# Kernel tuning notes

Measured on AMD Instinct MI355X. Metric: run time of the kernel, lower is better.

Reference implementation:

```python
import jax, jax.numpy as jnp
import numpy as np

GRID = 16
K = 2
NW = (GRID - K + 1) ** 2  # 225 sliding 2x2 windows on the 16x16 grid


def _make_mask():
    idx = np.arange(GRID * GRID).reshape(GRID, GRID)
    wins = np.stack([idx[i:i + K, j:j + K].ravel()
                     for i in range(GRID - K + 1) for j in range(GRID - K + 1)])
    m = np.zeros((NW, GRID * GRID), np.float32)
    m[np.arange(NW)[:, None], wins] = 1.0
    return jnp.asarray(m)

MASK = _make_mask()          # [225, 256] window -> covered cells
MASK_COUNT = MASK.sum(0)     # windows covering each cell
BN_SCALE = np.float32(1.0 / np.sqrt(1.0 + 1e-5))  # eval BN, running mean=0 var=1


def _adapter(x, w1, w2):
    return jax.nn.relu(jax.nn.relu(x @ w1.T) @ w2.T)


def _bn(x, g, b):
    return x * (g * BN_SCALE) + b


def _head(x, w1, b1, g2, be2, w2, b2, g3, be3, w3, b3):
    x = _bn(jax.nn.relu(x @ w1.T + b1), g2, be2)
    x = _bn(jax.nn.relu(x @ w2.T + b2), g3, be3)
    return jax.nn.sigmoid(x @ w3.T + b3)[:, 0]


def setup_inputs() -> dict:
    B, L, P, D, R, S = 64, 3, 225, 640, 1800, 240
    key = jax.random.key(0)
    ks = jax.random.split(key, 16)
    n = lambda k, s, sc=1.0: jax.random.normal(k, s, jnp.float32) * sc
    te = n(ks[3], (2, D)); te = te / jnp.linalg.norm(te, axis=-1, keepdims=True)
    pr = n(ks[5], (L, R, D)); pr = pr / jnp.linalg.norm(pr, axis=-1, keepdims=True)
    w = 0.05
    return dict(
        image=n(ks[0], (B, 3, S, S)),
        image_embeds=n(ks[1], (B, D)),
        patch_embeds=n(ks[2], (L, B, P, D)),
        text_embeds=te,
        image_embeds_ref=n(ks[4], (1, D)),
        patch_embeds_ref=pr,
        a_w1=n(ks[6], (160, D), w), a_w2=n(ks[7], (D, 160), w),
        r_w1=n(ks[8], (128, D), w), r_b1=jnp.zeros((128,)),
        r_g2=jnp.ones((128,)), r_be2=jnp.zeros((128,)),
        r_w2=n(ks[9], (64, 128), w), r_b2=jnp.zeros((64,)),
        r_g3=jnp.ones((64,)), r_be3=jnp.zeros((64,)),
        r_w3=n(ks[10], (1, 64), w), r_b3=jnp.zeros((1,)),
        h_w1=n(ks[11], (128, P), w), h_b1=jnp.zeros((128,)),
        h_g2=jnp.ones((128,)), h_be2=jnp.zeros((128,)),
        h_w2=n(ks[12], (64, 128), w), h_b2=jnp.zeros((64,)),
        h_g3=jnp.ones((64,)), h_be3=jnp.zeros((64,)),
        h_w3=n(ks[13], (1, 64), w), h_b3=jnp.zeros((1,)),
    )


def reference(image, image_embeds, patch_embeds, text_embeds, image_embeds_ref,
              patch_embeds_ref, a_w1, a_w2,
              r_w1, r_b1, r_g2, r_be2, r_w2, r_b2, r_g3, r_be3, r_w3, r_b3,
              h_w1, h_b1, h_g2, h_be2, h_w2, h_b2, h_g3, h_be3, h_w3, h_b3):
    pe = patch_embeds / jnp.linalg.norm(patch_embeds, axis=-1, keepdims=True)
    nie = image_embeds / jnp.linalg.norm(image_embeds, axis=-1, keepdims=True)
    text_score = jax.nn.softmax(100.0 * nie @ text_embeds.T, axis=-1)[:, 1]
    # kNN-style min-distance over reference patches: [L,B,P,R]
    sim = jnp.einsum('lbpd,lrd->lbpr', pe, patch_embeds_ref)
    patch_ref_map = ((1.0 - sim).min(axis=3) / 2.0).mean(axis=0)  # [B,P]
    fg_score = patch_ref_map.max(axis=1)
    diff = image_embeds_ref - _adapter(image_embeds, a_w1, a_w2)
    img_ref_score = _head(diff, r_w1, r_b1, r_g2, r_be2, r_w2, r_b2, r_g3, r_be3, r_w3, r_b3)
    holistic = (text_score + img_ref_score)[:, None] + patch_ref_map  # [B,225]
    hl_score = _head(holistic, h_w1, h_b1, h_g2, h_be2, h_w2, h_b2, h_g3, h_be3, h_w3, h_b3)
    final_score = (hl_score + fg_score) / 2.0
    # harmonic aggregation of window scores onto the 16x16 grid
    heat = (MASK_COUNT / ((1.0 / holistic) @ MASK)).reshape(-1, GRID, GRID)
    hmap = jax.image.resize(heat, (heat.shape[0], image.shape[2], image.shape[3]), 'bilinear')
    return final_score, hmap
```

## Files before the change

kernel.cpp:

```cpp
#include <hip/hip_runtime.h>
#include <stdint.h>
#include <math.h>

#define L_DIM 3
#define B_DIM 64
#define P_DIM 225
#define D_DIM 640
#define R_DIM 1800
#define S_DIM 240
#define M_TOT 14400
#define M_PAD 14592
#define N_PAD 2048
#define MT 57
#define NT 8
#define KT 10
#define BNSCALE 0.99999500003749981f

typedef __bf16 bf16x8 __attribute__((ext_vector_type(8)));
typedef float f32x4 __attribute__((ext_vector_type(4)));

__device__ __forceinline__ unsigned short f2bf(float f) {
    union { float f; unsigned u; } v; v.f = f;
    unsigned u = v.u;
    unsigned r = (u + 0x7FFFu + ((u >> 16) & 1u)) >> 16;
    return (unsigned short)r;
}

__global__ __launch_bounds__(256)
void k_convert(const float* __restrict__ pe, const float* __restrict__ per,
               unsigned short* __restrict__ abf, unsigned short* __restrict__ rbf,
               float* __restrict__ rnorm)
{
    const int AROWS = L_DIM * M_PAD;
    int wid = (blockIdx.x * 256 + threadIdx.x) >> 6;
    int lane = threadIdx.x & 63;
    const ushort4 z4 = {0, 0, 0, 0};
    if (wid < AROWS) {
        int l = wid / M_PAD, r = wid - l * M_PAD;
        unsigned short* dst = abf + (size_t)wid * D_DIM;
        if (r < M_TOT) {
            const float4* src = (const float4*)(pe + ((size_t)l * M_TOT + r) * D_DIM);
            float ss = 0.f;
            #pragma unroll
            for (int it = 0; it < 3; ++it) {
                int idx = it * 64 + lane;
                if (idx < 160) {
                    float4 v = src[idx];
                    ss += v.x * v.x + v.y * v.y + v.z * v.z + v.w * v.w;
                    ushort4 o;
                    o.x = f2bf(v.x); o.y = f2bf(v.y); o.z = f2bf(v.z); o.w = f2bf(v.w);
                    *(ushort4*)(dst + idx * 4) = o;
                }
            }
            #pragma unroll
            for (int m = 32; m; m >>= 1) ss += __shfl_xor(ss, m);
            if (lane == 0) rnorm[l * M_TOT + r] = rsqrtf(ss);
        } else {
            #pragma unroll
            for (int it = 0; it < 3; ++it) {
                int idx = it * 64 + lane;
                if (idx < 160) *(ushort4*)(dst + idx * 4) = z4;
            }
        }
    } else {
        int w2 = wid - AROWS;
        int l = w2 / N_PAD, r = w2 - l * N_PAD;
        unsigned short* dst = rbf + (size_t)w2 * D_DIM;
        if (r < R_DIM) {
            const float4* src = (const float4*)(per + ((size_t)l * R_DIM + r) * D_DIM);
            #pragma unroll
            for (int it = 0; it < 3; ++it) {
                int idx = it * 64 + lane;
                if (idx < 160) {
                    float4 v = src[idx];
                    ushort4 o;
                    o.x = f2bf(v.x); o.y = f2bf(v.y); o.z = f2bf(v.z); o.w = f2bf(v.w);
                    *(ushort4*)(dst + idx * 4) = o;
                }
            }
        } else {
            #pragma unroll
            for (int it = 0; it < 3; ++it) {
                int idx = it * 64 + lane;
                if (idx < 160) *(ushort4*)(dst + idx * 4) = z4;
            }
        }
    }
}

#define MFMA(A, B, C) __builtin_amdgcn_mfma_f32_16x16x32_bf16((A), (B), (C), 0, 0, 0)
#define GLL(SRC, DSTOFF)                                                     \
    __builtin_amdgcn_global_load_lds(                                        \
        (const __attribute__((address_space(1))) void*)(SRC),               \
        (__attribute__((address_space(3))) void*)(lds + (DSTOFF)), 16, 0, 0)

#define RD_BQ(D0, D1, D2, D3, Q, BASE) do {                                  \
    D0 = *(const bf16x8*)(lds + (BASE) + (brow0 + (Q) * 32) * 64 + sw0);     \
    D1 = *(const bf16x8*)(lds + (BASE) + (brow0 + (Q) * 32) * 64 + sw1);     \
    D2 = *(const bf16x8*)(lds + (BASE) + (brow0 + (Q) * 32 + 16) * 64 + sw0);\
    D3 = *(const bf16x8*)(lds + (BASE) + (brow0 + (Q) * 32 + 16) * 64 + sw1);\
} while (0)

#define RD_A(BASE) do { _Pragma("unroll")                                    \
    for (int mi = 0; mi < 4; ++mi) {                                         \
        a[mi][0] = *(const bf16x8*)(lds + (BASE) + (arow0 + mi * 16) * 64 + sw0); \
        a[mi][1] = *(const bf16x8*)(lds + (BASE) + (arow0 + mi * 16) * 64 + sw1); \
    } } while (0)

#define MM(NJB, B0, B1, B2, B3) do { _Pragma("unroll")                       \
    for (int mi = 0; mi < 4; ++mi) {                                         \
        acc[mi][NJB]     = MFMA(a[mi][0], B0, acc[mi][NJB]);                 \
        acc[mi][NJB]     = MFMA(a[mi][1], B1, acc[mi][NJB]);                 \
        acc[mi][NJB + 1] = MFMA(a[mi][0], B2, acc[mi][NJB + 1]);             \
        acc[mi][NJB + 1] = MFMA(a[mi][1], B3, acc[mi][NJB + 1]);             \
    } } while (0)

__global__ __launch_bounds__(512, 2)
void k_gemm_max(const unsigned short* __restrict__ abf,
                const unsigned short* __restrict__ rbf,
                float* __restrict__ pmax)
{
    __shared__ unsigned short lds[65536];
    __shared__ float red[2][256];

    int bid = blockIdx.x;
    int v = (bid & 7) * 171 + (bid >> 3);
    int l = v / (MT * NT);
    int rem = v - l * (MT * NT);
    int mt = rem >> 3;
    int nt = rem & 7;

    int tid = threadIdx.x;
    int wid = tid >> 6, lane = tid & 63;
    int wm = wid >> 1;
    int wn = wid & 1;
    int lane15 = lane & 15, lg = lane >> 4;
    int sA = lane15 & 7;
    int sw0 = ((lg) ^ sA) << 3;
    int sw1 = ((4 + lg) ^ sA) << 3;
    int arow0 = wm * 64 + lane15;
    int brow0 = wn * 128 + lane15;

    int rowc = lane >> 3;
    int scol = ((lane & 7) ^ rowc) << 3;
    const unsigned short* gA = abf + (size_t)(l * M_PAD + mt * 256) * D_DIM;
    const unsigned short* gB = rbf + (size_t)(l * N_PAD + nt * 256) * D_DIM;
    int chA0 = wid, chA1 = 8 + wid, chA2 = 16 + wid, chA3 = 24 + wid;
    int chB0 = (wid < 4) ? (0 + wid) : (12 + wid);
    int chB1 = (wid < 4) ? (4 + wid) : (16 + wid);
    int chB2 = (wid < 4) ? (8 + wid) : (20 + wid);
    int chB3 = (wid < 4) ? (12 + wid) : (24 + wid);
    const unsigned short* pA0 = gA + (size_t)(chA0 * 8 + rowc) * D_DIM + scol;
    const unsigned short* pA1 = gA + (size_t)(chA1 * 8 + rowc) * D_DIM + scol;
    const unsigned short* pA2 = gA + (size_t)(chA2 * 8 + rowc) * D_DIM + scol;
    const unsigned short* pA3 = gA + (size_t)(chA3 * 8 + rowc) * D_DIM + scol;
    const unsigned short* pB0 = gB + (size_t)(chB0 * 8 + rowc) * D_DIM + scol;
    const unsigned short* pB1 = gB + (size_t)(chB1 * 8 + rowc) * D_DIM + scol;
    const unsigned short* pB2 = gB + (size_t)(chB2 * 8 + rowc) * D_DIM + scol;
    const unsigned short* pB3 = gB + (size_t)(chB3 * 8 + rowc) * D_DIM + scol;

    f32x4 acc[4][8];
    #pragma unroll
    for (int mi = 0; mi < 4; ++mi)
        #pragma unroll
        for (int nj = 0; nj < 8; ++nj)
            acc[mi][nj] = f32x4{0.f, 0.f, 0.f, 0.f};

    GLL(pA0, chA0 * 512); GLL(pA1, chA1 * 512);
    GLL(pA2, chA2 * 512); GLL(pA3, chA3 * 512);
    GLL(pB0, 32768 + chB0 * 512); GLL(pB1, 32768 + chB1 * 512);
    GLL(pB2, 32768 + chB2 * 512); GLL(pB3, 32768 + chB3 * 512);
    asm volatile("s_waitcnt vmcnt(3)" ::: "memory");
    __builtin_amdgcn_s_barrier();

    bf16x8 a[4][2];
    bf16x8 ba0, ba1, ba2, ba3, bb0, bb1, bb2, bb3;
    RD_A(0);
    RD_BQ(ba0, ba1, ba2, ba3, 0, 32768);

    int buf = 0;
    for (int kt = 0; kt < KT; ++kt) {
        int ob = buf ^ 1;
        int bB = 32768 + buf * 16384;
        int oaB = ob * 16384;
        int obB = 32768 + ob * 16384;
        int koff = (kt + 1 < KT ? kt + 1 : KT - 1) * 64;

        GLL(pA0 + koff, oaB + chA0 * 512); GLL(pA1 + koff, oaB + chA1 * 512);
        asm volatile("s_waitcnt vmcnt(4)" ::: "memory");
        __builtin_amdgcn_s_barrier();
        RD_BQ(bb0, bb1, bb2, bb3, 1, bB);
        __builtin_amdgcn_s_setprio(1);
        MM(0, ba0, ba1, ba2, ba3);
        __builtin_amdgcn_s_setprio(0);

        GLL(pA2 + koff, oaB + chA2 * 512); GLL(pA3 + koff, oaB + chA3 * 512);
        asm volatile("s_waitcnt vmcnt(5)" ::: "memory");
        __builtin_amdgcn_s_barrier();
        RD_BQ(ba0, ba1, ba2, ba3, 2, bB);
        __builtin_amdgcn_s_setprio(1);
        MM(2, bb0, bb1, bb2, bb3);
        __builtin_amdgcn_s_setprio(0);

        GLL(pB0 + koff, obB + chB0 * 512); GLL(pB1 + koff, obB + chB1 * 512);
        asm volatile("s_waitcnt vmcnt(6)" ::: "memory");
        __builtin_amdgcn_s_barrier();
        RD_BQ(bb0, bb1, bb2, bb3, 3, bB);
        __builtin_amdgcn_s_setprio(1);
        MM(4, ba0, ba1, ba2, ba3);
        __builtin_amdgcn_s_setprio(0);

        GLL(pB2 + koff, obB + chB2 * 512); GLL(pB3 + koff, obB + chB3 * 512);
        asm volatile("s_waitcnt vmcnt(3)" ::: "memory");
        __builtin_amdgcn_s_barrier();
        RD_A(oaB);
        RD_BQ(ba0, ba1, ba2, ba3, 0, obB);
        __builtin_amdgcn_s_setprio(1);
        MM(6, bb0, bb1, bb2, bb3);
        __builtin_amdgcn_s_setprio(0);

        buf = ob;
    }

    __syncthreads();

    int colbase = nt * 256 + wn * 128 + lane15;
    #pragma unroll
    for (int mi = 0; mi < 4; ++mi) {
        float t[4] = {-__builtin_inff(), -__builtin_inff(),
                      -__builtin_inff(), -__builtin_inff()};
        #pragma unroll
        for (int nj = 0; nj < 8; ++nj) {
            if (colbase + nj * 16 < R_DIM) {
                #pragma unroll
                for (int r = 0; r < 4; ++r) t[r] = fmaxf(t[r], acc[mi][nj][r]);
            }
        }
        #pragma unroll
        for (int m = 1; m <= 8; m <<= 1) {
            #pragma unroll
            for (int r = 0; r < 4; ++r) t[r] = fmaxf(t[r], __shfl_xor(t[r], m));
        }
        if (lane15 == 0) {
            int rb = wm * 64 + mi * 16 + lg * 4;
            #pragma unroll
            for (int r = 0; r < 4; ++r) red[wn][rb + r] = t[r];
        }
    }
    __syncthreads();
    if (tid < 256) {
        float vmx = fmaxf(red[0][tid], red[1][tid]);
        pmax[((size_t)l * NT + nt) * M_PAD + mt * 256 + tid] = vmx;
    }
}

__device__ __forceinline__ float block_sum8(float v, volatile float* scratch) {
    #pragma unroll
    for (int m = 32; m; m >>= 1) v += __shfl_xor(v, m);
    int w = threadIdx.x >> 6;
    __syncthreads();
    if ((threadIdx.x & 63) == 0) scratch[w] = v;
    __syncthreads();
    float r = 0.f;
    #pragma unroll
    for (int i = 0; i < 8; ++i) r += scratch[i];
    return r;
}
__device__ __forceinline__ float block_max8(float v, volatile float* scratch) {
    #pragma unroll
    for (int m = 32; m; m >>= 1) v = fmaxf(v, __shfl_xor(v, m));
    int w = threadIdx.x >> 6;
    __syncthreads();
    if ((threadIdx.x & 63) == 0) scratch[w] = v;
    __syncthreads();
    float r = scratch[0];
    #pragma unroll
    for (int i = 1; i < 8; ++i) r = fmaxf(r, scratch[i]);
    return r;
}

__global__ __launch_bounds__(512)
void k_small(const float* __restrict__ ie, const float* __restrict__ te,
             const float* __restrict__ ier,
             const float* __restrict__ a_w1, const float* __restrict__ a_w2,
             const float* __restrict__ r_w1, const float* __restrict__ r_b1,
             const float* __restrict__ r_g2, const float* __restrict__ r_be2,
             const float* __restrict__ r_w2, const float* __restrict__ r_b2,
             const float* __restrict__ r_g3, const float* __restrict__ r_be3,
             const float* __restrict__ r_w3, const float* __restrict__ r_b3,
             const float* __restrict__ h_w1, const float* __restrict__ h_b1,
             const float* __restrict__ h_g2, const float* __restrict__ h_be2,
             const float* __restrict__ h_w2, const float* __restrict__ h_b2,
             const float* __restrict__ h_g3, const float* __restrict__ h_be3,
             const float* __restrict__ h_w3, const float* __restrict__ h_b3,
             const float* __restrict__ pmax, const float* __restrict__ rnorm,
             float* __restrict__ heat, float* __restrict__ out_score)
{
    int b = blockIdx.x, tid = threadIdx.x;
    __shared__ float x[D_DIM];
    __shared__ float h1[160];
    __shared__ float dif[D_DIM];
    __shared__ float z1[128];
    __shared__ float z2[64];
    __shared__ float hol[P_DIM];
    __shared__ float rcp[P_DIM];
    __shared__ float scratch[8];

    for (int i = tid; i < D_DIM; i += 512) x[i] = ie[b * D_DIM + i];
    __syncthreads();

    float ss = 0.f, d0 = 0.f, d1 = 0.f;
    for (int i = tid; i < D_DIM; i += 512) {
        float v = x[i];
        ss += v * v;
        d0 += v * te[i];
        d1 += v * te[D_DIM + i];
    }
    float ssum = block_sum8(ss, scratch);
    float dd0 = block_sum8(d0, scratch);
    float dd1 = block_sum8(d1, scratch);
    float tscore = 1.f / (1.f + expf(100.f * rsqrtf(ssum) * (dd0 - dd1)));

    for (int o = tid; o < 160; o += 512) {
        const float* w = a_w1 + (size_t)o * D_DIM;
        float s0 = 0, s1 = 0, s2 = 0, s3 = 0;
        for (int d = 0; d < D_DIM; d += 4) {
            s0 += x[d] * w[d]; s1 += x[d + 1] * w[d + 1];
            s2 += x[d + 2] * w[d + 2]; s3 += x[d + 3] * w[d + 3];
        }
        h1[o] = fmaxf((s0 + s1) + (s2 + s3), 0.f);
    }
    __syncthreads();
    for (int d = tid; d < D_DIM; d += 512) {
        const float* w = a_w2 + (size_t)d * 160;
        float s0 = 0, s1 = 0, s2 = 0, s3 = 0;
        for (int o = 0; o < 160; o += 4) {
            s0 += h1[o] * w[o]; s1 += h1[o + 1] * w[o + 1];
            s2 += h1[o + 2] * w[o + 2]; s3 += h1[o + 3] * w[o + 3];
        }
        dif[d] = ier[d] - fmaxf((s0 + s1) + (s2 + s3), 0.f);
    }
    __syncthreads();

    for (int o = tid; o < 128; o += 512) {
        const float* w = r_w1 + (size_t)o * D_DIM;
        float s0 = 0, s1 = 0, s2 = 0, s3 = 0;
        for (int d = 0; d < D_DIM; d += 4) {
            s0 += dif[d] * w[d]; s1 += dif[d + 1] * w[d + 1];
            s2 += dif[d + 2] * w[d + 2]; s3 += dif[d + 3] * w[d + 3];
        }
        float s = (s0 + s1) + (s2 + s3) + r_b1[o];
        z1[o] = fmaxf(s, 0.f) * (r_g2[o] * BNSCALE) + r_be2[o];
    }
    __syncthreads();
    for (int o = tid; o < 64; o += 512) {
        const float* w = r_w2 + (size_t)o * 128;
        float s = r_b2[o];
        for (int d = 0; d < 128; ++d) s += z1[d] * w[d];
        z2[o] = fmaxf(s, 0.f) * (r_g3[o] * BNSCALE) + r_be3[o];
    }
    __syncthreads();
    float sp = (tid < 64) ? z2[tid] * r_w3[tid] : 0.f;
    float irs = 1.f / (1.f + expf(-(block_sum8(sp, scratch) + r_b3[0])));

    float fgp = -__builtin_inff();
    float base = tscore + irs;
    for (int p = tid; p < P_DIM; p += 512) {
        int r = b * P_DIM + p;
        float s = 0.f;
        #pragma unroll
        for (int l = 0; l < L_DIM; ++l) {
            float m = -__builtin_inff();
            #pragma unroll
            for (int t = 0; t < NT; ++t)
                m = fmaxf(m, pmax[((size_t)l * NT + t) * M_PAD + r]);
            s += m * rnorm[l * M_TOT + r];
        }
        float pv = (3.0f - s) / 6.0f;
        fgp = fmaxf(fgp, pv);
        float h = base + pv;
        hol[p] = h;
        rcp[p] = 1.f / h;
    }
    float fg = block_max8(fgp, scratch);

    for (int o = tid; o < 128; o += 512) {
        const float* w = h_w1 + (size_t)o * P_DIM;
        float s = h_b1[o];
        for (int d = 0; d < P_DIM; ++d) s += hol[d] * w[d];
        z1[o] = fmaxf(s, 0.f) * (h_g2[o] * BNSCALE) + h_be2[o];
    }
    __syncthreads();
    for (int o = tid; o < 64; o += 512) {
        const float* w = h_w2 + (size_t)o * 128;
        float s = h_b2[o];
        for (int d = 0; d < 128; ++d) s += z1[d] * w[d];
        z2[o] = fmaxf(s, 0.f) * (h_g3[o] * BNSCALE) + h_be3[o];
    }
    __syncthreads();
    float sp2 = (tid < 64) ? z2[tid] * h_w3[tid] : 0.f;
    float hl_in = block_sum8(sp2, scratch) + h_b3[0];
    if (tid == 0) {
        float hl = 1.f / (1.f + expf(-hl_in));
        out_score[b] = (hl + fg) * 0.5f;
    }

    if (tid < 256) {
        int r = tid >> 4, c = tid & 15;
        float s = 0.f, cnt = 0.f;
        #pragma unroll
        for (int di = -1; di <= 0; ++di) {
            int i = r + di;
            if (i < 0 || i > 14) continue;
            #pragma unroll
            for (int dj = -1; dj <= 0; ++dj) {
                int j = c + dj;
                if (j < 0 || j > 14) continue;
                s += rcp[i * 15 + j];
                cnt += 1.f;
            }
        }
        heat[b * 256 + tid] = cnt / s;
    }
}

__global__ __launch_bounds__(256)
void k_resize(const float* __restrict__ heat, float* __restrict__ outh)
{
    int b = blockIdx.x >> 3, sub = blockIdx.x & 7;
    __shared__ float h[256];
    if (threadIdx.x < 256) h[threadIdx.x] = heat[b * 256 + threadIdx.x];
    __syncthreads();
    int base = sub * 30 * S_DIM;
    for (int q = threadIdx.x; q < 30 * S_DIM; q += 256) {
        int px = base + q;
        int y = px / S_DIM, xc = px - y * S_DIM;
        float sy = fminf(fmaxf((y - 7) * (1.0f / 15.0f), 0.f), 15.f);
        float sx = fminf(fmaxf((xc - 7) * (1.0f / 15.0f), 0.f), 15.f);
        int y0 = (int)sy, x0 = (int)sx;
        int y1 = min(y0 + 1, 15), x1 = min(x0 + 1, 15);
        float fy = sy - (float)y0, fx = sx - (float)x0;
        float v00 = h[y0 * 16 + x0], v01 = h[y0 * 16 + x1];
        float v10 = h[y1 * 16 + x0], v11 = h[y1 * 16 + x1];
        float v = (1.f - fy) * ((1.f - fx) * v00 + fx * v01)
                + fy * ((1.f - fx) * v10 + fx * v11);
        outh[(size_t)b * (S_DIM * S_DIM) + px] = v;
    }
}

extern "C" void kernel_launch(void* const* d_in, const int* in_sizes, int n_in,
                              void* d_out, int out_size, void* d_ws, size_t ws_size,
                              hipStream_t stream)
{
    (void)in_sizes; (void)n_in; (void)out_size; (void)ws_size;
    const float* image_embeds = (const float*)d_in[1];
    const float* patch_embeds = (const float*)d_in[2];
    const float* text_embeds  = (const float*)d_in[3];
    const float* ier          = (const float*)d_in[4];
    const float* per          = (const float*)d_in[5];
    const float* a_w1 = (const float*)d_in[6];
    const float* a_w2 = (const float*)d_in[7];
    const float* r_w1 = (const float*)d_in[8];
    const float* r_b1 = (const float*)d_in[9];
    const float* r_g2 = (const float*)d_in[10];
    const float* r_be2 = (const float*)d_in[11];
    const float* r_w2 = (const float*)d_in[12];
    const float* r_b2 = (const float*)d_in[13];
    const float* r_g3 = (const float*)d_in[14];
    const float* r_be3 = (const float*)d_in[15];
    const float* r_w3 = (const float*)d_in[16];
    const float* r_b3 = (const float*)d_in[17];
    const float* h_w1 = (const float*)d_in[18];
    const float* h_b1 = (const float*)d_in[19];
    const float* h_g2 = (const float*)d_in[20];
    const float* h_be2 = (const float*)d_in[21];
    const float* h_w2 = (const float*)d_in[22];
    const float* h_b2 = (const float*)d_in[23];
    const float* h_g3 = (const float*)d_in[24];
    const float* h_be3 = (const float*)d_in[25];
    const float* h_w3 = (const float*)d_in[26];
    const float* h_b3 = (const float*)d_in[27];

    char* ws = (char*)d_ws;
    size_t off = 0;
    auto take = [&](size_t bytes) -> void* {
        void* p = ws + off;
        off += (bytes + 255) & ~(size_t)255;
        return p;
    };
    float* rnorm = (float*)take((size_t)L_DIM * M_TOT * 4);
    float* pmax  = (float*)take((size_t)L_DIM * NT * M_PAD * 4);
    float* heat  = (float*)take((size_t)B_DIM * 256 * 4);
    unsigned short* abf = (unsigned short*)take((size_t)L_DIM * M_PAD * D_DIM * 2);
    unsigned short* rbf = (unsigned short*)take((size_t)L_DIM * N_PAD * D_DIM * 2);

    float* out_f = (float*)d_out;

    k_convert<<<dim3((L_DIM * M_PAD + L_DIM * N_PAD) / 4), dim3(256), 0, stream>>>(
        patch_embeds, per, abf, rbf, rnorm);
    k_gemm_max<<<dim3(L_DIM * MT * NT), dim3(512), 0, stream>>>(abf, rbf, pmax);
    k_small<<<dim3(B_DIM), dim3(512), 0, stream>>>(image_embeds, text_embeds, ier,
        a_w1, a_w2, r_w1, r_b1, r_g2, r_be2, r_w2, r_b2, r_g3, r_be3, r_w3, r_b3,
        h_w1, h_b1, h_g2, h_be2, h_w2, h_b2, h_g3, h_be3, h_w3, h_b3,
        pmax, rnorm, heat, out_f);
    k_resize<<<dim3(B_DIM * 8), dim3(256), 0, stream>>>(heat, out_f + B_DIM);
}
```

Before: 212.4 us.

## Restructure GEMM k-loop into two half-stages and fuse resize into k_small

```diff
diff --git a/kernel.cpp b/kernel.cpp
--- a/kernel.cpp
+++ b/kernel.cpp
@@ -94,11 +94,11 @@
         (const __attribute__((address_space(1))) void*)(SRC),               \
         (__attribute__((address_space(3))) void*)(lds + (DSTOFF)), 16, 0, 0)
 
-#define RD_BQ(D0, D1, D2, D3, Q, BASE) do {                                  \
-    D0 = *(const bf16x8*)(lds + (BASE) + (brow0 + (Q) * 32) * 64 + sw0);     \
-    D1 = *(const bf16x8*)(lds + (BASE) + (brow0 + (Q) * 32) * 64 + sw1);     \
-    D2 = *(const bf16x8*)(lds + (BASE) + (brow0 + (Q) * 32 + 16) * 64 + sw0);\
-    D3 = *(const bf16x8*)(lds + (BASE) + (brow0 + (Q) * 32 + 16) * 64 + sw1);\
+#define RD_Q(D, Q, BASE) do {                                                \
+    D[0] = *(const bf16x8*)(lds + (BASE) + (brow0 + (Q) * 32) * 64 + sw0);   \
+    D[1] = *(const bf16x8*)(lds + (BASE) + (brow0 + (Q) * 32) * 64 + sw1);   \
+    D[2] = *(const bf16x8*)(lds + (BASE) + (brow0 + (Q) * 32 + 16) * 64 + sw0); \
+    D[3] = *(const bf16x8*)(lds + (BASE) + (brow0 + (Q) * 32 + 16) * 64 + sw1); \
 } while (0)
 
 #define RD_A(BASE) do { _Pragma("unroll")                                    \
@@ -107,15 +107,15 @@
         a[mi][1] = *(const bf16x8*)(lds + (BASE) + (arow0 + mi * 16) * 64 + sw1); \
     } } while (0)
 
-#define MM(NJB, B0, B1, B2, B3) do { _Pragma("unroll")                       \
+#define MM(NJB, BQ) do { _Pragma("unroll")                                   \
     for (int mi = 0; mi < 4; ++mi) {                                         \
-        acc[mi][NJB]     = MFMA(a[mi][0], B0, acc[mi][NJB]);                 \
-        acc[mi][NJB]     = MFMA(a[mi][1], B1, acc[mi][NJB]);                 \
-        acc[mi][NJB + 1] = MFMA(a[mi][0], B2, acc[mi][NJB + 1]);             \
-        acc[mi][NJB + 1] = MFMA(a[mi][1], B3, acc[mi][NJB + 1]);             \
+        acc[mi][NJB]     = MFMA(a[mi][0], BQ[0], acc[mi][NJB]);              \
+        acc[mi][NJB]     = MFMA(a[mi][1], BQ[1], acc[mi][NJB]);              \
+        acc[mi][NJB + 1] = MFMA(a[mi][0], BQ[2], acc[mi][NJB + 1]);          \
+        acc[mi][NJB + 1] = MFMA(a[mi][1], BQ[3], acc[mi][NJB + 1]);          \
     } } while (0)
 
-__global__ __launch_bounds__(512, 2)
+__global__ __launch_bounds__(512, 1)
 void k_gemm_max(const unsigned short* __restrict__ abf,
                 const unsigned short* __restrict__ rbf,
                 float* __restrict__ pmax)
@@ -170,56 +170,62 @@
     GLL(pA2, chA2 * 512); GLL(pA3, chA3 * 512);
     GLL(pB0, 32768 + chB0 * 512); GLL(pB1, 32768 + chB1 * 512);
     GLL(pB2, 32768 + chB2 * 512); GLL(pB3, 32768 + chB3 * 512);
-    asm volatile("s_waitcnt vmcnt(3)" ::: "memory");
+    asm volatile("s_waitcnt vmcnt(2)" ::: "memory");
     __builtin_amdgcn_s_barrier();
 
-    bf16x8 a[4][2];
-    bf16x8 ba0, ba1, ba2, ba3, bb0, bb1, bb2, bb3;
-    RD_A(0);
-    RD_BQ(ba0, ba1, ba2, ba3, 0, 32768);
-
     int buf = 0;
-    for (int kt = 0; kt < KT; ++kt) {
+    for (int kt = 0; kt < KT - 1; ++kt) {
         int ob = buf ^ 1;
+        int aB = buf * 16384;
         int bB = 32768 + buf * 16384;
         int oaB = ob * 16384;
         int obB = 32768 + ob * 16384;
-        int koff = (kt + 1 < KT ? kt + 1 : KT - 1) * 64;
-
-        GLL(pA0 + koff, oaB + chA0 * 512); GLL(pA1 + koff, oaB + chA1 * 512);
-        asm volatile("s_waitcnt vmcnt(4)" ::: "memory");
+        int koff = (kt + 1) * 64;
+
+        bf16x8 a[4][2];
+        {
+            RD_A(aB);
+            bf16x8 q0[4], q1[4];
+            RD_Q(q0, 0, bB); RD_Q(q1, 1, bB);
+            GLL(pA0 + koff, oaB + chA0 * 512); GLL(pA1 + koff, oaB + chA1 * 512);
+            GLL(pA2 + koff, oaB + chA2 * 512); GLL(pA3 + koff, oaB + chA3 * 512);
+            asm volatile("s_waitcnt vmcnt(4)" ::: "memory");
+            __builtin_amdgcn_s_barrier();
+            __builtin_amdgcn_s_setprio(1);
+            MM(0, q0); MM(2, q1);
+            __builtin_amdgcn_s_setprio(0);
+        }
+        {
+            bf16x8 q2[4], q3[4];
+            RD_Q(q2, 2, bB); RD_Q(q3, 3, bB);
+            GLL(pB0 + koff, obB + chB0 * 512); GLL(pB1 + koff, obB + chB1 * 512);
+            GLL(pB2 + koff, obB + chB2 * 512); GLL(pB3 + koff, obB + chB3 * 512);
+            asm volatile("s_waitcnt vmcnt(2)" ::: "memory");
+            __builtin_amdgcn_s_barrier();
+            __builtin_amdgcn_s_setprio(1);
+            MM(4, q2); MM(6, q3);
+            __builtin_amdgcn_s_setprio(0);
+        }
+        buf = ob;
+    }
+
+    {
+        int aB = buf * 16384;
+        int bB = 32768 + buf * 16384;
+        bf16x8 a[4][2];
+        RD_A(aB);
+        bf16x8 q0[4], q1[4];
+        RD_Q(q0, 0, bB); RD_Q(q1, 1, bB);
+        asm volatile("s_waitcnt vmcnt(0)" ::: "memory");
         __builtin_amdgcn_s_barrier();
-        RD_BQ(bb0, bb1, bb2, bb3, 1, bB);
         __builtin_amdgcn_s_setprio(1);
-        MM(0, ba0, ba1, ba2, ba3);
+        MM(0, q0); MM(2, q1);
         __builtin_amdgcn_s_setprio(0);
-
-        GLL(pA2 + koff, oaB + chA2 * 512); GLL(pA3 + koff, oaB + chA3 * 512);
-        asm volatile("s_waitcnt vmcnt(5)" ::: "memory");
-        __builtin_amdgcn_s_barrier();
-        RD_BQ(ba0, ba1, ba2, ba3, 2, bB);
+        bf16x8 q2[4], q3[4];
+        RD_Q(q2, 2, bB); RD_Q(q3, 3, bB);
         __builtin_amdgcn_s_setprio(1);
-        MM(2, bb0, bb1, bb2, bb3);
+        MM(4, q2); MM(6, q3);
         __builtin_amdgcn_s_setprio(0);
-
-        GLL(pB0 + koff, obB + chB0 * 512); GLL(pB1 + koff, obB + chB1 * 512);
-        asm volatile("s_waitcnt vmcnt(6)" ::: "memory");
-        __builtin_amdgcn_s_barrier();
-        RD_BQ(bb0, bb1, bb2, bb3, 3, bB);
-        __builtin_amdgcn_s_setprio(1);
-        MM(4, ba0, ba1, ba2, ba3);
-        __builtin_amdgcn_s_setprio(0);
-
-        GLL(pB2 + koff, obB + chB2 * 512); GLL(pB3 + koff, obB + chB3 * 512);
-        asm volatile("s_waitcnt vmcnt(3)" ::: "memory");
-        __builtin_amdgcn_s_barrier();
-        RD_A(oaB);
-        RD_BQ(ba0, ba1, ba2, ba3, 0, obB);
-        __builtin_amdgcn_s_setprio(1);
-        MM(6, bb0, bb1, bb2, bb3);
-        __builtin_amdgcn_s_setprio(0);
-
-        buf = ob;
     }
 
     __syncthreads();
@@ -294,7 +300,7 @@
              const float* __restrict__ h_g3, const float* __restrict__ h_be3,
              const float* __restrict__ h_w3, const float* __restrict__ h_b3,
              const float* __restrict__ pmax, const float* __restrict__ rnorm,
-             float* __restrict__ heat, float* __restrict__ out_score)
+             float* __restrict__ out_score, float* __restrict__ outh)
 {
     int b = blockIdx.x, tid = threadIdx.x;
     __shared__ float x[D_DIM];
@@ -304,6 +310,7 @@
     __shared__ float z2[64];
     __shared__ float hol[P_DIM];
     __shared__ float rcp[P_DIM];
+    __shared__ float heatl[256];
     __shared__ float scratch[8];
 
     for (int i = tid; i < D_DIM; i += 512) x[i] = ie[b * D_DIM + i];
@@ -420,31 +427,23 @@
                 cnt += 1.f;
             }
         }
-        heat[b * 256 + tid] = cnt / s;
-    }
-}
-
-__global__ __launch_bounds__(256)
-void k_resize(const float* __restrict__ heat, float* __restrict__ outh)
-{
-    int b = blockIdx.x >> 3, sub = blockIdx.x & 7;
-    __shared__ float h[256];
-    if (threadIdx.x < 256) h[threadIdx.x] = heat[b * 256 + threadIdx.x];
-    __syncthreads();
-    int base = sub * 30 * S_DIM;
-    for (int q = threadIdx.x; q < 30 * S_DIM; q += 256) {
-        int px = base + q;
+        heatl[tid] = cnt / s;
+    }
+    __syncthreads();
+
+    float* dst = outh + (size_t)b * (S_DIM * S_DIM);
+    for (int px = tid; px < S_DIM * S_DIM; px += 512) {
         int y = px / S_DIM, xc = px - y * S_DIM;
         float sy = fminf(fmaxf((y - 7) * (1.0f / 15.0f), 0.f), 15.f);
         float sx = fminf(fmaxf((xc - 7) * (1.0f / 15.0f), 0.f), 15.f);
         int y0 = (int)sy, x0 = (int)sx;
         int y1 = min(y0 + 1, 15), x1 = min(x0 + 1, 15);
         float fy = sy - (float)y0, fx = sx - (float)x0;
-        float v00 = h[y0 * 16 + x0], v01 = h[y0 * 16 + x1];
-        float v10 = h[y1 * 16 + x0], v11 = h[y1 * 16 + x1];
-        float v = (1.f - fy) * ((1.f - fx) * v00 + fx * v01)
-                + fy * ((1.f - fx) * v10 + fx * v11);
-        outh[(size_t)b * (S_DIM * S_DIM) + px] = v;
+        float v00 = heatl[y0 * 16 + x0], v01 = heatl[y0 * 16 + x1];
+        float v10 = heatl[y1 * 16 + x0], v11 = heatl[y1 * 16 + x1];
+        float vv = (1.f - fy) * ((1.f - fx) * v00 + fx * v01)
+                 + fy * ((1.f - fx) * v10 + fx * v11);
+        dst[px] = vv;
     }
 }
 
@@ -490,7 +489,6 @@
     };
     float* rnorm = (float*)take((size_t)L_DIM * M_TOT * 4);
     float* pmax  = (float*)take((size_t)L_DIM * NT * M_PAD * 4);
-    float* heat  = (float*)take((size_t)B_DIM * 256 * 4);
     unsigned short* abf = (unsigned short*)take((size_t)L_DIM * M_PAD * D_DIM * 2);
     unsigned short* rbf = (unsigned short*)take((size_t)L_DIM * N_PAD * D_DIM * 2);
 
@@ -502,6 +500,5 @@
     k_small<<<dim3(B_DIM), dim3(512), 0, stream>>>(image_embeds, text_embeds, ier,
         a_w1, a_w2, r_w1, r_b1, r_g2, r_be2, r_w2, r_b2, r_g3, r_be3, r_w3, r_b3,
         h_w1, h_b1, h_g2, h_be2, h_w2, h_b2, h_g3, h_be3, h_w3, h_b3,
-        pmax, rnorm, heat, out_f);
-    k_resize<<<dim3(B_DIM * 8), dim3(256), 0, stream>>>(heat, out_f + B_DIM);
-}
+        pmax, rnorm, out_f, out_f + B_DIM);
+}
```

Result: no change. 214.6 us (+1.0%).
